# Kernel tuning notes

Measured on AMD Instinct MI355X. Metric: run time of the kernel, lower is better.

Reference implementation:

```python
import jax, jax.numpy as jnp
import numpy as np

B, N, CIN, K = 4, 4096, 64, 16
MLP = [64, 64, 128]
EPS = 1e-5


def setup_inputs() -> dict:
    key = jax.random.key(0)
    ks = jax.random.split(key, 8)
    inp = {
        "xyz": jax.random.normal(ks[0], (B, N, 3), dtype=jnp.float32),
        "points": jax.random.normal(ks[1], (B, N, CIN), dtype=jnp.float32),
    }
    last = 3 + CIN
    for i, oc in enumerate(MLP):
        inp[f"w{i}"] = jax.random.normal(ks[2 + i], (oc, last), dtype=jnp.float32) * 0.05
        inp[f"b{i}"] = jnp.zeros((oc,), dtype=jnp.float32)
        inp[f"g{i}"] = jnp.ones((oc,), dtype=jnp.float32)
        inp[f"be{i}"] = jnp.zeros((oc,), dtype=jnp.float32)
        inp[f"rm{i}"] = jnp.zeros((oc,), dtype=jnp.float32)
        inp[f"rv{i}"] = jnp.ones((oc,), dtype=jnp.float32)
        last = oc
    return inp


def reference(xyz, points, w0, b0, g0, be0, rm0, rv0,
              w1, b1, g1, be1, rm1, rv1,
              w2, b2, g2, be2, rm2, rv2):
    # knn via squared pairwise distance (same argsort order as cdist)
    sq = jnp.sum(xyz * xyz, axis=-1)  # (B,N)
    d2 = sq[:, :, None] + sq[:, None, :] - 2.0 * jnp.einsum('bnc,bmc->bnm', xyz, xyz)
    _, idx = jax.lax.top_k(-d2, K)  # (B,N,K), smallest-distance neighbors

    bidx = jnp.arange(xyz.shape[0])[:, None, None]  # (B,1,1)
    grouped_xyz = xyz[bidx, idx] - xyz[:, :, None, :]     # (B,N,K,3) relative coords
    grouped_pts = points[bidx, idx]                        # (B,N,K,CIN)
    h = jnp.concatenate([grouped_xyz, grouped_pts], axis=-1)  # (B,N,K,3+CIN)

    layers = [(w0, b0, g0, be0, rm0, rv0),
              (w1, b1, g1, be1, rm1, rv1),
              (w2, b2, g2, be2, rm2, rv2)]
    for (w, b, g, be, rm, rv) in layers:
        # 1x1 conv == per-point linear; BN in eval mode (running stats)
        h = jnp.einsum('bnkc,oc->bnko', h, w) + b
        h = (h - rm) * jax.lax.rsqrt(rv + EPS) * g + be
        h = jax.nn.relu(h)
    new_points = jnp.max(h, axis=2)  # max over K neighbors -> (B,N,C_out)
    return new_points
```

## Files before the change

### kernel.cpp

```cpp
#include <hip/hip_runtime.h>

#define NPT   4096
#define KNN_K 16
#define EPSV  1e-5f

#define W0T_OFF 0
#define B0_OFF  4288
#define W1T_OFF 4352
#define B1_OFF  8448
#define W2T_OFF 8512
#define B2_OFF  16704
#define IDX_OFF 16832
#define XYZ4_OFF 278976
#define P_OFF   344512
#define Q_OFF   1393088

typedef unsigned long long ull;

__global__ void prep_kernel(
    const float* __restrict__ xyz,
    const float* __restrict__ w0, const float* __restrict__ b0, const float* __restrict__ g0,
    const float* __restrict__ be0, const float* __restrict__ rm0, const float* __restrict__ rv0,
    const float* __restrict__ w1, const float* __restrict__ b1, const float* __restrict__ g1,
    const float* __restrict__ be1, const float* __restrict__ rm1, const float* __restrict__ rv1,
    const float* __restrict__ w2, const float* __restrict__ b2, const float* __restrict__ g2,
    const float* __restrict__ be2, const float* __restrict__ rm2, const float* __restrict__ rv2,
    float* __restrict__ ws) {
  int blk = blockIdx.x;
  if (blk < 64) {
    int i = blk * 256 + threadIdx.x;
    const float* p = xyz + i * 3;
    float x = p[0], y = p[1], z = p[2];
    float sq = __fadd_rn(__fadd_rn(__fmul_rn(x, x), __fmul_rn(y, y)), __fmul_rn(z, z));
    ((float4*)(ws + XYZ4_OFF))[i] = make_float4(x, y, z, sq);
    return;
  }
  int i = (blk - 64) * 256 + threadIdx.x;
  if (i < 4288) {
    int oc = i & 63, icp = i >> 6;
    int col = (icp < 64) ? (icp + 3) : (icp - 64);
    float s = g0[oc] * rsqrtf(rv0[oc] + EPSV);
    ws[W0T_OFF + i] = w0[oc * 67 + col] * s;
  } else if (i < 4352) {
    int oc = i - 4288;
    float s = g0[oc] * rsqrtf(rv0[oc] + EPSV);
    ws[i] = (b0[oc] - rm0[oc]) * s + be0[oc];
  } else if (i < 8448) {
    int j = i - 4352; int oc = j & 63, ic = j >> 6;
    float s = g1[oc] * rsqrtf(rv1[oc] + EPSV);
    ws[i] = w1[oc * 64 + ic] * s;
  } else if (i < 8512) {
    int oc = i - 8448;
    float s = g1[oc] * rsqrtf(rv1[oc] + EPSV);
    ws[i] = (b1[oc] - rm1[oc]) * s + be1[oc];
  } else if (i < 16704) {
    int j = i - 8512; int ic = j >> 7, oc = j & 127;
    float s = g2[oc] * rsqrtf(rv2[oc] + EPSV);
    ws[i] = w2[oc * 64 + ic] * s;
  } else if (i < 16832) {
    int oc = i - 16704;
    float s = g2[oc] * rsqrtf(rv2[oc] + EPSV);
    ws[i] = (b2[oc] - rm2[oc]) * s + be2[oc];
  }
}

__global__ __launch_bounds__(256) void pq_kernel(const float* __restrict__ xyz,
                                                 const float* __restrict__ points,
                                                 float* __restrict__ ws) {
  int tid = threadIdx.x;
  int oc = tid & 63;
  int i = blockIdx.x * 4 + (tid >> 6);
  const float* w0t = ws + W0T_OFF;
  float x = xyz[i * 3], y = xyz[i * 3 + 1], z = xyz[i * 3 + 2];
  float qacc = w0t[64 * 64 + oc] * x;
  qacc = fmaf(w0t[65 * 64 + oc], y, qacc);
  qacc = fmaf(w0t[66 * 64 + oc], z, qacc);
  float acc = ws[B0_OFF + oc] + qacc;
  const float* prow = points + (size_t)i * 64;
#pragma unroll 4
  for (int c = 0; c < 64; ++c) acc = fmaf(w0t[c * 64 + oc], prow[c], acc);
  ws[P_OFF + (size_t)i * 64 + oc] = acc;
  ws[Q_OFF + (size_t)i * 64 + oc] = qacc;
}

__device__ __forceinline__ ull minu64(ull a, ull b) { return a < b ? a : b; }
__device__ __forceinline__ ull maxu64(ull a, ull b) { return a > b ? a : b; }

__device__ __forceinline__ ull bitonic_sort64(ull v, int lane) {
#pragma unroll
  for (int k = 2; k <= 64; k <<= 1) {
#pragma unroll
    for (int j = k >> 1; j > 0; j >>= 1) {
      ull o = __shfl_xor(v, j);
      bool lower = (lane & j) == 0;
      bool up = (lane & k) == 0;
      v = (lower == up) ? minu64(v, o) : maxu64(v, o);
    }
  }
  return v;
}

__device__ __forceinline__ ull bitonic_merge64(ull v, int lane) {
#pragma unroll
  for (int j = 32; j > 0; j >>= 1) {
    ull o = __shfl_xor(v, j);
    v = ((lane & j) == 0) ? minu64(v, o) : maxu64(v, o);
  }
  return v;
}

__global__ __launch_bounds__(256) void knn_kernel(const float4* __restrict__ cand4,
                                                  int* __restrict__ knnOut) {
  __shared__ __align__(16) float4 tile[1024];
  __shared__ ull buf[4][128];
  int tid = threadIdx.x;
  int lane = tid & 63, w = tid >> 6;
  int b = blockIdx.x >> 10;
  int n = ((blockIdx.x & 1023) << 2) + w;
  const float4* cb = cand4 + b * NPT;

  float4 q = cb[n];
  ull R = ~0ull;
  ull thresh = ~0ull;
  int cnt = 0;
  ull ltmask = (lane == 0) ? 0ull : (~0ull >> (64 - lane));

#pragma unroll 1
  for (int t = 0; t < 4; ++t) {
    __syncthreads();
#pragma unroll
    for (int j = 0; j < 4; ++j) tile[j * 256 + tid] = cb[t * 1024 + j * 256 + tid];
    __syncthreads();
#pragma unroll 1
    for (int i = 0; i < 16; ++i) {
      int ml = (i << 6) + lane;
      float4 c = tile[ml];
      float dot = __fadd_rn(__fadd_rn(__fmul_rn(q.x, c.x), __fmul_rn(q.y, c.y)),
                            __fmul_rn(q.z, c.z));
      float d2 = __fsub_rn(__fadd_rn(q.w, c.w), __fmul_rn(2.0f, dot));
      unsigned bits = __float_as_uint(d2);
      unsigned fk = bits ^ (0x80000000u | (unsigned)((int)bits >> 31));
      ull key = ((ull)fk << 32) | (unsigned)((t << 10) + ml);
      bool pred = key < thresh;
      ull mask = __ballot(pred);
      if (mask) {
        int pos = cnt + __popcll(mask & ltmask);
        if (pred) buf[w][pos] = key;
        cnt += __popcll(mask);
        if (cnt >= 64) {
          ull v = buf[w][lane];
          v = bitonic_sort64(v, lane);
          ull vr = __shfl(v, 63 - lane);
          R = minu64(R, vr);
          R = bitonic_merge64(R, lane);
          thresh = __shfl(R, 15);
          cnt -= 64;
          if (lane < cnt) {
            ull tmp = buf[w][64 + lane];
            buf[w][lane] = tmp;
          }
        }
      }
    }
  }
  {
    ull v = (lane < cnt) ? buf[w][lane] : ~0ull;
    v = bitonic_sort64(v, lane);
    ull vr = __shfl(v, 63 - lane);
    R = minu64(R, vr);
    R = bitonic_merge64(R, lane);
  }
  if (lane < KNN_K)
    knnOut[(b * NPT + n) * KNN_K + lane] = (int)(unsigned)(R & 0xFFFFFFFFull);
}

__global__ __launch_bounds__(256) void mlp_kernel(
    const float* __restrict__ wbuf, const int* __restrict__ knn,
    float* __restrict__ out) {
  __shared__ __align__(16) float Ash[4][64 * 32];
  __shared__ __align__(16) float W1lds[64 * 64];
  __shared__ __align__(16) float W2lds[64 * 128];
  int tid = threadIdx.x;
  int lane = tid & 63, w = tid >> 6;
  int c = lane & 7, r = lane >> 3;
  int b = blockIdx.x >> 9;
  int qbase = ((blockIdx.x & 511) << 3) + (w << 1);

  {
    const float4* w1s = (const float4*)(wbuf + W1T_OFF);
    float4* w1d = (float4*)W1lds;
#pragma unroll
    for (int t = 0; t < 4; ++t) w1d[t * 256 + tid] = w1s[t * 256 + tid];
    const float4* w2s = (const float4*)(wbuf + W2T_OFF);
    float4* w2d = (float4*)W2lds;
#pragma unroll
    for (int t = 0; t < 8; ++t) w2d[t * 256 + tid] = w2s[t * 256 + tid];
  }

  {
    int p = lane >> 1, half = lane & 1;
    int q = qbase + (p >> 4), k = p & 15;
    int src = knn[(b * NPT + q) * KNN_K + k];
    const float4* Pp = (const float4*)(wbuf + P_OFF + ((size_t)(b * NPT + src) * 64 + half * 32));
    const float4* Qp = (const float4*)(wbuf + Q_OFF + ((size_t)(b * NPT + q) * 64 + half * 32));
    float* Aw = Ash[w];
#pragma unroll
    for (int j = 0; j < 8; ++j) {
      float4 pv = Pp[j];
      float4 qv = Qp[j];
      int ic = half * 32 + j * 4;
      Aw[(ic + 0) * 32 + p] = fmaxf(pv.x - qv.x, 0.0f);
      Aw[(ic + 1) * 32 + p] = fmaxf(pv.y - qv.y, 0.0f);
      Aw[(ic + 2) * 32 + p] = fmaxf(pv.z - qv.z, 0.0f);
      Aw[(ic + 3) * 32 + p] = fmaxf(pv.w - qv.w, 0.0f);
    }
  }
  __syncthreads();

  float* Aw = Ash[w];
  float acc[4][8];

#pragma unroll
  for (int j = 0; j < 8; ++j) {
    float bv = wbuf[B1_OFF + 8 * c + j];
#pragma unroll
    for (int i = 0; i < 4; ++i) acc[i][j] = bv;
  }
#pragma unroll 4
  for (int ic = 0; ic < 64; ++ic) {
    float4 a4 = *(const float4*)(Aw + ic * 32 + 4 * r);
    float4 w40 = *(const float4*)(W1lds + ic * 64 + 8 * c);
    float4 w41 = *(const float4*)(W1lds + ic * 64 + 8 * c + 4);
    float av[4] = {a4.x, a4.y, a4.z, a4.w};
    float wv[8] = {w40.x, w40.y, w40.z, w40.w, w41.x, w41.y, w41.z, w41.w};
#pragma unroll
    for (int i = 0; i < 4; ++i)
#pragma unroll
      for (int j = 0; j < 8; ++j) acc[i][j] = fmaf(av[i], wv[j], acc[i][j]);
  }
  __builtin_amdgcn_wave_barrier();
#pragma unroll
  for (int j = 0; j < 8; ++j) {
    int oc = 8 * c + j;
    float4 v = make_float4(fmaxf(acc[0][j], 0.0f), fmaxf(acc[1][j], 0.0f),
                           fmaxf(acc[2][j], 0.0f), fmaxf(acc[3][j], 0.0f));
    *(float4*)(Aw + oc * 32 + 4 * r) = v;
  }
  __builtin_amdgcn_wave_barrier();

  int qout = qbase + (lane >> 5);
  bool storer = (lane & 31) < 8;
  float* obase = out + ((size_t)(b * NPT + qout) * 128 + 8 * c);
#pragma unroll 1
  for (int pass = 0; pass < 2; ++pass) {
#pragma unroll
    for (int j = 0; j < 8; ++j) {
      float bv = wbuf[B2_OFF + pass * 64 + 8 * c + j];
#pragma unroll
      for (int i = 0; i < 4; ++i) acc[i][j] = bv;
    }
#pragma unroll 4
    for (int ic = 0; ic < 64; ++ic) {
      float4 a4 = *(const float4*)(Aw + ic * 32 + 4 * r);
      const float* wrow = W2lds + ic * 128 + pass * 64 + 8 * c;
      float4 w40 = *(const float4*)(wrow);
      float4 w41 = *(const float4*)(wrow + 4);
      float av[4] = {a4.x, a4.y, a4.z, a4.w};
      float wv[8] = {w40.x, w40.y, w40.z, w40.w, w41.x, w41.y, w41.z, w41.w};
#pragma unroll
      for (int i = 0; i < 4; ++i)
#pragma unroll
        for (int j = 0; j < 8; ++j) acc[i][j] = fmaf(av[i], wv[j], acc[i][j]);
    }
    float m[8];
#pragma unroll
    for (int j = 0; j < 8; ++j) {
      float v = fmaxf(fmaxf(acc[0][j], acc[1][j]), fmaxf(acc[2][j], acc[3][j]));
      v = fmaxf(v, 0.0f);
      v = fmaxf(v, __shfl_xor(v, 8));
      v = fmaxf(v, __shfl_xor(v, 16));
      m[j] = v;
    }
    if (storer) {
      *(float4*)(obase + pass * 64)     = make_float4(m[0], m[1], m[2], m[3]);
      *(float4*)(obase + pass * 64 + 4) = make_float4(m[4], m[5], m[6], m[7]);
    }
  }
}

extern "C" void kernel_launch(void* const* d_in, const int* in_sizes, int n_in,
                              void* d_out, int out_size, void* d_ws, size_t ws_size,
                              hipStream_t stream) {
  const float* xyz    = (const float*)d_in[0];
  const float* points = (const float*)d_in[1];
  float* wsF = (float*)d_ws;
  int* idxBuf = (int*)(wsF + IDX_OFF);
  const float4* cand4 = (const float4*)(wsF + XYZ4_OFF);

  prep_kernel<<<130, 256, 0, stream>>>(
      xyz,
      (const float*)d_in[2],  (const float*)d_in[3],  (const float*)d_in[4],
      (const float*)d_in[5],  (const float*)d_in[6],  (const float*)d_in[7],
      (const float*)d_in[8],  (const float*)d_in[9],  (const float*)d_in[10],
      (const float*)d_in[11], (const float*)d_in[12], (const float*)d_in[13],
      (const float*)d_in[14], (const float*)d_in[15], (const float*)d_in[16],
      (const float*)d_in[17], (const float*)d_in[18], (const float*)d_in[19],
      wsF);
  pq_kernel<<<4096, 256, 0, stream>>>(xyz, points, wsF);
  knn_kernel<<<4096, 256, 0, stream>>>(cand4, idxBuf);
  mlp_kernel<<<2048, 256, 0, stream>>>(wsF, idxBuf, (float*)d_out);
}
```

Before: 277.2 us.

## Restructure MLP kernel to one neighbor row per lane with scalar-broadcast weights

The MLP kernel now maps each lane to one (query, neighbor) row and keeps all 64 output channels in registers. Weights are read straight from global memory at wave-uniform addresses, which can become scalar loads, instead of being staged in LDS. Each block now covers 16 queries, so the grid is halved. This removes the LDS weight staging, the block-wide sync and the LDS weight reads. In exchange it raises register pressure to about 64+ accumulators per lane, which may lower occupancy, and adds more shuffle reductions across the 16 neighbors.

```diff
diff --git a/kernel.cpp b/kernel.cpp
--- a/kernel.cpp
+++ b/kernel.cpp
@@ -177,113 +177,78 @@
 __global__ __launch_bounds__(256) void mlp_kernel(
     const float* __restrict__ wbuf, const int* __restrict__ knn,
     float* __restrict__ out) {
-  __shared__ __align__(16) float Ash[4][64 * 32];
-  __shared__ __align__(16) float W1lds[64 * 64];
-  __shared__ __align__(16) float W2lds[64 * 128];
+  __shared__ float Ash[4][64 * 64];
   int tid = threadIdx.x;
   int lane = tid & 63, w = tid >> 6;
-  int c = lane & 7, r = lane >> 3;
-  int b = blockIdx.x >> 9;
-  int qbase = ((blockIdx.x & 511) << 3) + (w << 1);
+  float* Aw = Ash[w];
+
+  int q = blockIdx.x * 16 + w * 4 + (lane >> 4);
+  int k = lane & 15;
+  int src = knn[q * KNN_K + k];
+  int srow = (q & ~(NPT - 1)) + src;
 
   {
-    const float4* w1s = (const float4*)(wbuf + W1T_OFF);
-    float4* w1d = (float4*)W1lds;
-#pragma unroll
-    for (int t = 0; t < 4; ++t) w1d[t * 256 + tid] = w1s[t * 256 + tid];
-    const float4* w2s = (const float4*)(wbuf + W2T_OFF);
-    float4* w2d = (float4*)W2lds;
-#pragma unroll
-    for (int t = 0; t < 8; ++t) w2d[t * 256 + tid] = w2s[t * 256 + tid];
-  }
-
-  {
-    int p = lane >> 1, half = lane & 1;
-    int q = qbase + (p >> 4), k = p & 15;
-    int src = knn[(b * NPT + q) * KNN_K + k];
-    const float4* Pp = (const float4*)(wbuf + P_OFF + ((size_t)(b * NPT + src) * 64 + half * 32));
-    const float4* Qp = (const float4*)(wbuf + Q_OFF + ((size_t)(b * NPT + q) * 64 + half * 32));
-    float* Aw = Ash[w];
-#pragma unroll
-    for (int j = 0; j < 8; ++j) {
+    const float4* Pp = (const float4*)(wbuf + P_OFF + (size_t)srow * 64);
+    const float4* Qp = (const float4*)(wbuf + Q_OFF + (size_t)q * 64);
+#pragma unroll
+    for (int j = 0; j < 16; ++j) {
       float4 pv = Pp[j];
       float4 qv = Qp[j];
-      int ic = half * 32 + j * 4;
-      Aw[(ic + 0) * 32 + p] = fmaxf(pv.x - qv.x, 0.0f);
-      Aw[(ic + 1) * 32 + p] = fmaxf(pv.y - qv.y, 0.0f);
-      Aw[(ic + 2) * 32 + p] = fmaxf(pv.z - qv.z, 0.0f);
-      Aw[(ic + 3) * 32 + p] = fmaxf(pv.w - qv.w, 0.0f);
-    }
-  }
-  __syncthreads();
-
-  float* Aw = Ash[w];
-  float acc[4][8];
-
-#pragma unroll
-  for (int j = 0; j < 8; ++j) {
-    float bv = wbuf[B1_OFF + 8 * c + j];
-#pragma unroll
-    for (int i = 0; i < 4; ++i) acc[i][j] = bv;
-  }
-#pragma unroll 4
-  for (int ic = 0; ic < 64; ++ic) {
-    float4 a4 = *(const float4*)(Aw + ic * 32 + 4 * r);
-    float4 w40 = *(const float4*)(W1lds + ic * 64 + 8 * c);
-    float4 w41 = *(const float4*)(W1lds + ic * 64 + 8 * c + 4);
-    float av[4] = {a4.x, a4.y, a4.z, a4.w};
-    float wv[8] = {w40.x, w40.y, w40.z, w40.w, w41.x, w41.y, w41.z, w41.w};
-#pragma unroll
-    for (int i = 0; i < 4; ++i)
-#pragma unroll
-      for (int j = 0; j < 8; ++j) acc[i][j] = fmaf(av[i], wv[j], acc[i][j]);
+      int ic = j * 4;
+      Aw[(ic + 0) * 64 + lane] = fmaxf(pv.x - qv.x, 0.0f);
+      Aw[(ic + 1) * 64 + lane] = fmaxf(pv.y - qv.y, 0.0f);
+      Aw[(ic + 2) * 64 + lane] = fmaxf(pv.z - qv.z, 0.0f);
+      Aw[(ic + 3) * 64 + lane] = fmaxf(pv.w - qv.w, 0.0f);
+    }
   }
   __builtin_amdgcn_wave_barrier();
-#pragma unroll
-  for (int j = 0; j < 8; ++j) {
-    int oc = 8 * c + j;
-    float4 v = make_float4(fmaxf(acc[0][j], 0.0f), fmaxf(acc[1][j], 0.0f),
-                           fmaxf(acc[2][j], 0.0f), fmaxf(acc[3][j], 0.0f));
-    *(float4*)(Aw + oc * 32 + 4 * r) = v;
+
+  float h1[64];
+#pragma unroll
+  for (int j = 0; j < 64; ++j) h1[j] = wbuf[B1_OFF + j];
+  {
+    const float* w1 = wbuf + W1T_OFF;
+#pragma unroll 1
+    for (int ic = 0; ic < 64; ++ic) {
+      float a = Aw[ic * 64 + lane];
+      const float* wr = w1 + ic * 64;
+#pragma unroll
+      for (int j = 0; j < 64; ++j) h1[j] = fmaf(a, wr[j], h1[j]);
+    }
   }
   __builtin_amdgcn_wave_barrier();
-
-  int qout = qbase + (lane >> 5);
-  bool storer = (lane & 31) < 8;
-  float* obase = out + ((size_t)(b * NPT + qout) * 128 + 8 * c);
+#pragma unroll
+  for (int j = 0; j < 64; ++j) Aw[j * 64 + lane] = fmaxf(h1[j], 0.0f);
+  __builtin_amdgcn_wave_barrier();
+
+  const float* w2 = wbuf + W2T_OFF;
+  float* obase = out + (size_t)q * 128;
 #pragma unroll 1
   for (int pass = 0; pass < 2; ++pass) {
-#pragma unroll
-    for (int j = 0; j < 8; ++j) {
-      float bv = wbuf[B2_OFF + pass * 64 + 8 * c + j];
-#pragma unroll
-      for (int i = 0; i < 4; ++i) acc[i][j] = bv;
-    }
-#pragma unroll 4
+    float acc[64];
+#pragma unroll
+    for (int j = 0; j < 64; ++j) acc[j] = wbuf[B2_OFF + pass * 64 + j];
+#pragma unroll 1
     for (int ic = 0; ic < 64; ++ic) {
-      float4 a4 = *(const float4*)(Aw + ic * 32 + 4 * r);
-      const float* wrow = W2lds + ic * 128 + pass * 64 + 8 * c;
-      float4 w40 = *(const float4*)(wrow);
-      float4 w41 = *(const float4*)(wrow + 4);
-      float av[4] = {a4.x, a4.y, a4.z, a4.w};
-      float wv[8] = {w40.x, w40.y, w40.z, w40.w, w41.x, w41.y, w41.z, w41.w};
-#pragma unroll
-      for (int i = 0; i < 4; ++i)
-#pragma unroll
-        for (int j = 0; j < 8; ++j) acc[i][j] = fmaf(av[i], wv[j], acc[i][j]);
-    }
-    float m[8];
-#pragma unroll
-    for (int j = 0; j < 8; ++j) {
-      float v = fmaxf(fmaxf(acc[0][j], acc[1][j]), fmaxf(acc[2][j], acc[3][j]));
-      v = fmaxf(v, 0.0f);
+      float a = Aw[ic * 64 + lane];
+      const float* wr = w2 + ic * 128 + pass * 64;
+#pragma unroll
+      for (int j = 0; j < 64; ++j) acc[j] = fmaf(a, wr[j], acc[j]);
+    }
+#pragma unroll
+    for (int j = 0; j < 64; ++j) {
+      float v = fmaxf(acc[j], 0.0f);
+      v = fmaxf(v, __shfl_xor(v, 1));
+      v = fmaxf(v, __shfl_xor(v, 2));
+      v = fmaxf(v, __shfl_xor(v, 4));
       v = fmaxf(v, __shfl_xor(v, 8));
-      v = fmaxf(v, __shfl_xor(v, 16));
-      m[j] = v;
-    }
-    if (storer) {
-      *(float4*)(obase + pass * 64)     = make_float4(m[0], m[1], m[2], m[3]);
-      *(float4*)(obase + pass * 64 + 4) = make_float4(m[4], m[5], m[6], m[7]);
+      acc[j] = v;
+    }
+    if (k == 0) {
+      float4* o4 = (float4*)(obase + pass * 64);
+#pragma unroll
+      for (int j = 0; j < 16; ++j)
+        o4[j] = make_float4(acc[4 * j], acc[4 * j + 1], acc[4 * j + 2], acc[4 * j + 3]);
     }
   }
 }
@@ -308,5 +273,5 @@
       wsF);
   pq_kernel<<<4096, 256, 0, stream>>>(xyz, points, wsF);
   knn_kernel<<<4096, 256, 0, stream>>>(cand4, idxBuf);
-  mlp_kernel<<<2048, 256, 0, stream>>>(wsF, idxBuf, (float*)d_out);
-}
+  mlp_kernel<<<1024, 256, 0, stream>>>(wsF, idxBuf, (float*)d_out);
+}
```

Result: slower. 314.7 us (+13.5%).
